# Kernel tuning notes

Hardware: AMD Instinct MI355X
Metric: run time of the kernel (lower is better)

## Reference

```python
import jax, jax.numpy as jnp
import numpy as np

N = 50000
E = 800000
NODE_DIM = 128
EDGE_DIM = 64


def leaky_relu(x, slope=0.2):
    return jnp.where(x >= 0, x, slope * x)


def setup_inputs() -> dict:
    key = jax.random.key(0)
    ks = jax.random.split(key, 12)
    node_feats = jax.random.normal(ks[0], (N, NODE_DIM), dtype=jnp.float32)
    edge_index = jax.random.randint(ks[1], (2, E), 0, N, dtype=jnp.int64)
    edge_feats = jax.random.normal(ks[2], (E, EDGE_DIM), dtype=jnp.float32)
    # msg_mlp: Linear(node+edge -> node), LeakyReLU(0.2), Linear(node -> node)
    s1 = 1.0 / np.sqrt(NODE_DIM + EDGE_DIM)
    s2 = 1.0 / np.sqrt(NODE_DIM)
    s3 = 1.0 / np.sqrt(2 * NODE_DIM)
    msg_w1 = jax.random.uniform(ks[3], (NODE_DIM + EDGE_DIM, NODE_DIM), jnp.float32, -s1, s1)
    msg_b1 = jax.random.uniform(ks[4], (NODE_DIM,), jnp.float32, -s1, s1)
    msg_w2 = jax.random.uniform(ks[5], (NODE_DIM, NODE_DIM), jnp.float32, -s2, s2)
    msg_b2 = jax.random.uniform(ks[6], (NODE_DIM,), jnp.float32, -s2, s2)
    # update_mlp: Linear(2*node -> node), LeakyReLU(0.2), Linear(node -> node)
    upd_w1 = jax.random.uniform(ks[7], (2 * NODE_DIM, NODE_DIM), jnp.float32, -s3, s3)
    upd_b1 = jax.random.uniform(ks[8], (NODE_DIM,), jnp.float32, -s3, s3)
    upd_w2 = jax.random.uniform(ks[9], (NODE_DIM, NODE_DIM), jnp.float32, -s2, s2)
    upd_b2 = jax.random.uniform(ks[10], (NODE_DIM,), jnp.float32, -s2, s2)
    return {
        "node_feats": node_feats,
        "edge_feats": edge_feats,
        "msg_w1": msg_w1, "msg_b1": msg_b1, "msg_w2": msg_w2, "msg_b2": msg_b2,
        "upd_w1": upd_w1, "upd_b1": upd_b1, "upd_w2": upd_w2, "upd_b2": upd_b2,
        "edge_index": edge_index,
    }


def reference(node_feats, edge_feats, msg_w1, msg_b1, msg_w2, msg_b2,
              upd_w1, upd_b1, upd_w2, upd_b2, edge_index):
    src = edge_index[0]
    dst = edge_index[1]
    # gather neighbor features, concat with edge features: (E, node+edge)
    msg_input = jnp.concatenate([node_feats[dst], edge_feats], axis=1)
    h = leaky_relu(msg_input @ msg_w1 + msg_b1)
    messages = h @ msg_w2 + msg_b2                       # (E, node_dim)
    # scatter-add messages to source nodes
    aggregated = jax.ops.segment_sum(messages, src, num_segments=node_feats.shape[0])
    update_input = jnp.concatenate([node_feats, aggregated], axis=1)  # (N, 2*node_dim)
    h2 = leaky_relu(update_input @ upd_w1 + upd_b1)
    return h2 @ upd_w2 + upd_b2                          # (N, node_dim)
```

## Files before the change

### kernel.cpp

```cpp
#include <hip/hip_runtime.h>
#include <hip/hip_bf16.h>

#define NNODES 50000
#define NEDGES 800000
#define NDIM   128
#define EDIM   64
#define K1     192
#define K2     256
#define NB     196

#define KP1 200
#define KPA 136
#define KPU 264
#define MSTR 132

typedef __attribute__((ext_vector_type(8))) short bf16x8;
typedef __attribute__((ext_vector_type(4))) short bf16x4;
typedef __attribute__((ext_vector_type(4))) float f32x4;

__device__ inline short f2bf(float f) {
  union { float f; unsigned u; } v; v.f = f;
  unsigned r = v.u + 0x7FFFu + ((v.u >> 16) & 1u);
  return (short)(r >> 16);
}

__device__ inline bf16x4 pack4(float4 v) {
  bf16x4 p;
  p[0] = f2bf(v.x); p[1] = f2bf(v.y); p[2] = f2bf(v.z); p[3] = f2bf(v.w);
  return p;
}

__global__ __launch_bounds__(256) void cvt_kernel(const float* __restrict__ src,
                                                  short* __restrict__ dst, int n) {
  int i = (blockIdx.x * 256 + threadIdx.x) * 4;
  if (i < n) {
    float4 v = *(const float4*)(src + i);
    *(bf16x4*)(dst + i) = pack4(v);
  }
}

__global__ __launch_bounds__(256) void wt_kernel(const float* __restrict__ w,
                                                 short* __restrict__ wt, int K) {
  int i = blockIdx.x * 256 + threadIdx.x;
  if (i < K * NDIM) {
    int k = i >> 7;
    int n = i & 127;
    wt[n * K + k] = f2bf(w[i]);
  }
}

__global__ __launch_bounds__(256) void hist_kernel(const int* __restrict__ eidx,
                                                   int* __restrict__ cnt) {
  int i = blockIdx.x * 256 + threadIdx.x;
  if (i < NEDGES) atomicAdd(&cnt[eidx[i]], 1);
}

__global__ __launch_bounds__(256) void scan_reduce_kernel(const int* __restrict__ cnt,
                                                          int* __restrict__ bsum) {
  __shared__ int sh[256];
  int tid = threadIdx.x;
  int i = blockIdx.x * 256 + tid;
  sh[tid] = (i < NNODES) ? cnt[i] : 0;
  __syncthreads();
#pragma unroll
  for (int off = 128; off > 0; off >>= 1) {
    if (tid < off) sh[tid] += sh[tid + off];
    __syncthreads();
  }
  if (tid == 0) bsum[blockIdx.x] = sh[0];
}

__global__ __launch_bounds__(256) void scan_top_kernel(const int* __restrict__ bsum,
                                                       int* __restrict__ bscan) {
  __shared__ int sh[256];
  int tid = threadIdx.x;
  int v = (tid < NB) ? bsum[tid] : 0;
  sh[tid] = v;
  __syncthreads();
#pragma unroll
  for (int off = 1; off < 256; off <<= 1) {
    int t = (tid >= off) ? sh[tid - off] : 0;
    __syncthreads();
    sh[tid] += t;
    __syncthreads();
  }
  bscan[tid] = sh[tid] - v;
}

__global__ __launch_bounds__(256) void scan_down_kernel(int* __restrict__ cnt,
                                                        const int* __restrict__ bscan,
                                                        int* __restrict__ row_ptr) {
  __shared__ int sh[256];
  int tid = threadIdx.x;
  int i = blockIdx.x * 256 + tid;
  int v = (i < NNODES) ? cnt[i] : 0;
  sh[tid] = v;
  __syncthreads();
#pragma unroll
  for (int off = 1; off < 256; off <<= 1) {
    int t = (tid >= off) ? sh[tid - off] : 0;
    __syncthreads();
    sh[tid] += t;
    __syncthreads();
  }
  if (i < NNODES) {
    row_ptr[i] = bscan[blockIdx.x] + (sh[tid] - v);
    cnt[i] = 0;
  }
}

__global__ __launch_bounds__(256) void permute_kernel(const int* __restrict__ eidx,
                                                      const int* __restrict__ row_ptr,
                                                      int* __restrict__ cnt,
                                                      int4* __restrict__ s_edges) {
  int e = blockIdx.x * 256 + threadIdx.x;
  if (e < NEDGES) {
    int s = eidx[e];
    int d = eidx[NEDGES + e];
    int pos = row_ptr[s] + atomicAdd(&cnt[s], 1);
    s_edges[pos] = make_int4(s, d, e, 0);
  }
}

__global__ __launch_bounds__(256, 6) void edge_kernel(const short* __restrict__ nf_bf,
                                                      const float* __restrict__ edge_feats,
                                                      const int4* __restrict__ s_edges,
                                                      const short* __restrict__ w1t,
                                                      const float* __restrict__ b1,
                                                      float* __restrict__ hagg) {
  __shared__ __align__(16) char SH[64 * KP1 * 2];
  __shared__ int srcs[64];
  __shared__ int dsts[64];
  __shared__ int eids[64];

  short* X = (short*)SH;
  float* M = (float*)SH;

  const int tid = threadIdx.x;
  const int e0 = blockIdx.x * 64;

  if (tid < 64) {
    int4 v = s_edges[e0 + tid];
    srcs[tid] = v.x;
    dsts[tid] = v.y;
    eids[tid] = v.z;
  }
  __syncthreads();

  {
    int r = tid >> 2, q = tid & 3;
    const bf16x8* np = (const bf16x8*)(nf_bf + (size_t)dsts[r] * NDIM) + q * 4;
    const float4* ep = (const float4*)(edge_feats + (size_t)eids[r] * EDIM) + q * 4;
    short* dpn = X + r * KP1 + q * 32;
    short* dpe = X + r * KP1 + NDIM + q * 16;
#pragma unroll
    for (int j = 0; j < 4; ++j) *(bf16x8*)(dpn + j * 8) = np[j];
#pragma unroll
    for (int j = 0; j < 4; ++j) *(bf16x4*)(dpe + j * 4) = pack4(ep[j]);
  }
  __syncthreads();

  const int lane = tid & 63;
  const int wv = tid >> 6;
  const int m16 = lane & 15;
  const int quad = lane >> 4;

  f32x4 acc[4][2];
#pragma unroll
  for (int mt = 0; mt < 4; ++mt)
#pragma unroll
    for (int nt = 0; nt < 2; ++nt)
      acc[mt][nt] = (f32x4){0.f, 0.f, 0.f, 0.f};

#pragma unroll
  for (int ks = 0; ks < 6; ++ks) {
    const int k0 = ks * 32 + quad * 8;
    bf16x8 b[2];
#pragma unroll
    for (int nt = 0; nt < 2; ++nt) {
      int n = wv * 32 + nt * 16 + m16;
      b[nt] = *(const bf16x8*)(w1t + n * K1 + k0);
    }
#pragma unroll
    for (int mt = 0; mt < 4; ++mt) {
      bf16x8 a = *(const bf16x8*)(X + (mt * 16 + m16) * KP1 + k0);
#pragma unroll
      for (int nt = 0; nt < 2; ++nt)
        acc[mt][nt] = __builtin_amdgcn_mfma_f32_16x16x32_bf16(a, b[nt], acc[mt][nt], 0, 0, 0);
    }
  }
  __syncthreads();

#pragma unroll
  for (int h = 0; h < 2; ++h) {
#pragma unroll
    for (int nt = 0; nt < 2; ++nt) {
      int col = wv * 32 + nt * 16 + m16;
      float bb = b1[col];
#pragma unroll
      for (int mt2 = 0; mt2 < 2; ++mt2) {
        int mt = h * 2 + mt2;
#pragma unroll
        for (int i = 0; i < 4; ++i) {
          float v = acc[mt][nt][i] + bb;
          v = v >= 0.f ? v : 0.2f * v;
          int lr = mt2 * 16 + quad * 4 + i;
          M[lr * MSTR + col] = v;
        }
      }
    }
    __syncthreads();
    {
      const int c = tid & 127;
      const int lr0 = (tid >> 7) * 16;
      const int g0 = h * 32 + lr0;
      float a = M[lr0 * MSTR + c];
      int prev = srcs[g0];
#pragma unroll 4
      for (int r = 1; r < 16; ++r) {
        int s = srcs[g0 + r];
        float v = M[(lr0 + r) * MSTR + c];
        if (s != prev) {
          atomicAdd(&hagg[(size_t)prev * NDIM + c], a);
          a = v;
          prev = s;
        } else {
          a += v;
        }
      }
      atomicAdd(&hagg[(size_t)prev * NDIM + c], a);
    }
    if (h == 0) __syncthreads();
  }
}

__global__ __launch_bounds__(256) void node_kernel(const short* __restrict__ nf_bf,
                                                   const float* __restrict__ hagg,
                                                   const int* __restrict__ degc,
                                                   const short* __restrict__ w2t,
                                                   const float* __restrict__ b2,
                                                   const short* __restrict__ u1t,
                                                   const float* __restrict__ ub1,
                                                   const short* __restrict__ u2t,
                                                   const float* __restrict__ ub2,
                                                   float* __restrict__ out) {
  __shared__ __align__(16) short AGH[64 * KPA];
  __shared__ __align__(16) short XU[64 * KPU];
  __shared__ float degs[64];

  const int tid = threadIdx.x;
  const int n0 = blockIdx.x * 64;

  if (tid < 64) {
    int node = n0 + tid;
    degs[tid] = (node < NNODES) ? (float)degc[node] : 0.f;
  }
  {
    int r = tid >> 2, q = tid & 3;
    int node = n0 + r; if (node >= NNODES) node = NNODES - 1;
    const float4* hp = (const float4*)(hagg + (size_t)node * NDIM) + q * 8;
    const bf16x8* xp = (const bf16x8*)(nf_bf + (size_t)node * NDIM) + q * 4;
    short* ap = AGH + r * KPA + q * 32;
    short* xq = XU + r * KPU + q * 32;
#pragma unroll
    for (int j = 0; j < 8; ++j) *(bf16x4*)(ap + j * 4) = pack4(hp[j]);
#pragma unroll
    for (int j = 0; j < 4; ++j) *(bf16x8*)(xq + j * 8) = xp[j];
  }
  __syncthreads();

  const int lane = tid & 63;
  const int wv = tid >> 6;
  const int m16 = lane & 15;
  const int quad = lane >> 4;

  f32x4 acc[4][2];

#pragma unroll
  for (int mt = 0; mt < 4; ++mt)
#pragma unroll
    for (int nt = 0; nt < 2; ++nt)
      acc[mt][nt] = (f32x4){0.f, 0.f, 0.f, 0.f};
#pragma unroll
  for (int ks = 0; ks < 4; ++ks) {
    const int k0 = ks * 32 + quad * 8;
    bf16x8 b[2];
#pragma unroll
    for (int nt = 0; nt < 2; ++nt) {
      int n = wv * 32 + nt * 16 + m16;
      b[nt] = *(const bf16x8*)(w2t + n * NDIM + k0);
    }
#pragma unroll
    for (int mt = 0; mt < 4; ++mt) {
      bf16x8 a = *(const bf16x8*)(AGH + (mt * 16 + m16) * KPA + k0);
#pragma unroll
      for (int nt = 0; nt < 2; ++nt)
        acc[mt][nt] = __builtin_amdgcn_mfma_f32_16x16x32_bf16(a, b[nt], acc[mt][nt], 0, 0, 0);
    }
  }
#pragma unroll
  for (int nt = 0; nt < 2; ++nt) {
    int col = wv * 32 + nt * 16 + m16;
    float bb = b2[col];
#pragma unroll
    for (int mt = 0; mt < 4; ++mt) {
#pragma unroll
      for (int i = 0; i < 4; ++i) {
        int row = mt * 16 + quad * 4 + i;
        float v = acc[mt][nt][i] + degs[row] * bb;
        XU[row * KPU + NDIM + col] = f2bf(v);
      }
    }
  }
  __syncthreads();

#pragma unroll
  for (int mt = 0; mt < 4; ++mt)
#pragma unroll
    for (int nt = 0; nt < 2; ++nt)
      acc[mt][nt] = (f32x4){0.f, 0.f, 0.f, 0.f};
#pragma unroll
  for (int ks = 0; ks < 8; ++ks) {
    const int k0 = ks * 32 + quad * 8;
    bf16x8 b[2];
#pragma unroll
    for (int nt = 0; nt < 2; ++nt) {
      int n = wv * 32 + nt * 16 + m16;
      b[nt] = *(const bf16x8*)(u1t + n * K2 + k0);
    }
#pragma unroll
    for (int mt = 0; mt < 4; ++mt) {
      bf16x8 a = *(const bf16x8*)(XU + (mt * 16 + m16) * KPU + k0);
#pragma unroll
      for (int nt = 0; nt < 2; ++nt)
        acc[mt][nt] = __builtin_amdgcn_mfma_f32_16x16x32_bf16(a, b[nt], acc[mt][nt], 0, 0, 0);
    }
  }
  __syncthreads();
#pragma unroll
  for (int nt = 0; nt < 2; ++nt) {
    int col = wv * 32 + nt * 16 + m16;
    float bb = ub1[col];
#pragma unroll
    for (int mt = 0; mt < 4; ++mt) {
#pragma unroll
      for (int i = 0; i < 4; ++i) {
        int row = mt * 16 + quad * 4 + i;
        float v = acc[mt][nt][i] + bb;
        v = v >= 0.f ? v : 0.2f * v;
        AGH[row * KPA + col] = f2bf(v);
      }
    }
  }
  __syncthreads();

#pragma unroll
  for (int mt = 0; mt < 4; ++mt)
#pragma unroll
    for (int nt = 0; nt < 2; ++nt)
      acc[mt][nt] = (f32x4){0.f, 0.f, 0.f, 0.f};
#pragma unroll
  for (int ks = 0; ks < 4; ++ks) {
    const int k0 = ks * 32 + quad * 8;
    bf16x8 b[2];
#pragma unroll
    for (int nt = 0; nt < 2; ++nt) {
      int n = wv * 32 + nt * 16 + m16;
      b[nt] = *(const bf16x8*)(u2t + n * NDIM + k0);
    }
#pragma unroll
    for (int mt = 0; mt < 4; ++mt) {
      bf16x8 a = *(const bf16x8*)(AGH + (mt * 16 + m16) * KPA + k0);
#pragma unroll
      for (int nt = 0; nt < 2; ++nt)
        acc[mt][nt] = __builtin_amdgcn_mfma_f32_16x16x32_bf16(a, b[nt], acc[mt][nt], 0, 0, 0);
    }
  }
#pragma unroll
  for (int nt = 0; nt < 2; ++nt) {
    int col = wv * 32 + nt * 16 + m16;
    float bb = ub2[col];
#pragma unroll
    for (int mt = 0; mt < 4; ++mt) {
#pragma unroll
      for (int i = 0; i < 4; ++i) {
        int row = mt * 16 + quad * 4 + i;
        int node = n0 + row;
        if (node < NNODES)
          out[(size_t)node * NDIM + col] = acc[mt][nt][i] + bb;
      }
    }
  }
}

extern "C" void kernel_launch(void* const* d_in, const int* in_sizes, int n_in,
                              void* d_out, int out_size, void* d_ws, size_t ws_size,
                              hipStream_t stream) {
  const float* node_feats = (const float*)d_in[0];
  const float* edge_feats = (const float*)d_in[1];
  const float* msg_w1 = (const float*)d_in[2];
  const float* msg_b1 = (const float*)d_in[3];
  const float* msg_w2 = (const float*)d_in[4];
  const float* msg_b2 = (const float*)d_in[5];
  const float* upd_w1 = (const float*)d_in[6];
  const float* upd_b1 = (const float*)d_in[7];
  const float* upd_w2 = (const float*)d_in[8];
  const float* upd_b2 = (const float*)d_in[9];
  const int* eidx = (const int*)d_in[10];

  float* hagg   = (float*)d_ws;
  int* cnt      = (int*)(hagg + (size_t)NNODES * NDIM);
  int* row_ptr  = cnt + NNODES;
  int* bsum     = row_ptr + NNODES;
  int* bscan    = bsum + 256;
  int4* s_edges = (int4*)(bscan + 256);
  short* w1t    = (short*)(s_edges + NEDGES);
  short* w2t    = w1t + 128 * K1;
  short* u1t    = w2t + 128 * 128;
  short* u2t    = u1t + 128 * K2;
  short* nf_bf  = u2t + 128 * 128;

  hipMemsetAsync(d_ws, 0, (size_t)(NNODES * NDIM + NNODES) * sizeof(float), stream);

  cvt_kernel<<<(NNODES * NDIM / 4 + 255) / 256, 256, 0, stream>>>(node_feats, nf_bf,
                                                                  NNODES * NDIM);
  wt_kernel<<<(K1 * 128) / 256, 256, 0, stream>>>(msg_w1, w1t, K1);
  wt_kernel<<<(128 * 128) / 256, 256, 0, stream>>>(msg_w2, w2t, 128);
  wt_kernel<<<(K2 * 128) / 256, 256, 0, stream>>>(upd_w1, u1t, K2);
  wt_kernel<<<(128 * 128) / 256, 256, 0, stream>>>(upd_w2, u2t, 128);

  hist_kernel<<<NEDGES / 256, 256, 0, stream>>>(eidx, cnt);
  scan_reduce_kernel<<<NB, 256, 0, stream>>>(cnt, bsum);
  scan_top_kernel<<<1, 256, 0, stream>>>(bsum, bscan);
  scan_down_kernel<<<NB, 256, 0, stream>>>(cnt, bscan, row_ptr);
  permute_kernel<<<NEDGES / 256, 256, 0, stream>>>(eidx, row_ptr, cnt, s_edges);

  edge_kernel<<<NEDGES / 64, 256, 0, stream>>>(nf_bf, edge_feats, s_edges,
                                               w1t, msg_b1, hagg);
  node_kernel<<<(NNODES + 63) / 64, 256, 0, stream>>>(nf_bf, hagg, cnt,
                                                      w2t, msg_b2, u1t, upd_b1,
                                                      u2t, upd_b2, (float*)d_out);
}
```

Before: 541.1 us.

## Make edge kernel wave-independent with direct global A-fragment loads

Restructures the edge kernel so each wave owns 32 edges and all 128 output columns. The gathered node and edge features are loaded straight from global memory into MFMA A-fragments, with edge features converted to bf16 in registers, instead of being staged through a shared-memory X tile. Block-wide __syncthreads are replaced with per-wave barriers and an LDS waitcnt. The segmented scatter-add then runs per wave, with each lane handling two columns. This drops the LDS staging and block-level syncs, but doubles the accumulator registers, lowers the occupancy hint from 6 to 3, and makes each wave reload all of W1 from global memory or cache.

```diff
diff --git a/kernel.cpp b/kernel.cpp
--- a/kernel.cpp
+++ b/kernel.cpp
@@ -9,10 +9,11 @@
 #define K2     256
 #define NB     196
 
-#define KP1 200
 #define KPA 136
 #define KPU 264
 #define MSTR 132
+
+#define WAIT_LGKM 0xC07F
 
 typedef __attribute__((ext_vector_type(8))) short bf16x8;
 typedef __attribute__((ext_vector_type(4))) short bf16x4;
@@ -27,6 +28,13 @@
 __device__ inline bf16x4 pack4(float4 v) {
   bf16x4 p;
   p[0] = f2bf(v.x); p[1] = f2bf(v.y); p[2] = f2bf(v.z); p[3] = f2bf(v.w);
+  return p;
+}
+
+__device__ inline bf16x8 pack8(float4 a, float4 b) {
+  bf16x8 p;
+  p[0] = f2bf(a.x); p[1] = f2bf(a.y); p[2] = f2bf(a.z); p[3] = f2bf(a.w);
+  p[4] = f2bf(b.x); p[5] = f2bf(b.y); p[6] = f2bf(b.z); p[7] = f2bf(b.w);
   return p;
 }
 
@@ -122,115 +130,100 @@
   }
 }
 
-__global__ __launch_bounds__(256, 6) void edge_kernel(const short* __restrict__ nf_bf,
+__global__ __launch_bounds__(256, 3) void edge_kernel(const short* __restrict__ nf_bf,
                                                       const float* __restrict__ edge_feats,
                                                       const int4* __restrict__ s_edges,
                                                       const short* __restrict__ w1t,
                                                       const float* __restrict__ b1,
                                                       float* __restrict__ hagg) {
-  __shared__ __align__(16) char SH[64 * KP1 * 2];
-  __shared__ int srcs[64];
-  __shared__ int dsts[64];
-  __shared__ int eids[64];
-
-  short* X = (short*)SH;
-  float* M = (float*)SH;
+  __shared__ __align__(16) float M[4][16 * MSTR];
+  __shared__ int srcs[4][32];
 
   const int tid = threadIdx.x;
-  const int e0 = blockIdx.x * 64;
-
-  if (tid < 64) {
-    int4 v = s_edges[e0 + tid];
-    srcs[tid] = v.x;
-    dsts[tid] = v.y;
-    eids[tid] = v.z;
-  }
-  __syncthreads();
-
-  {
-    int r = tid >> 2, q = tid & 3;
-    const bf16x8* np = (const bf16x8*)(nf_bf + (size_t)dsts[r] * NDIM) + q * 4;
-    const float4* ep = (const float4*)(edge_feats + (size_t)eids[r] * EDIM) + q * 4;
-    short* dpn = X + r * KP1 + q * 32;
-    short* dpe = X + r * KP1 + NDIM + q * 16;
-#pragma unroll
-    for (int j = 0; j < 4; ++j) *(bf16x8*)(dpn + j * 8) = np[j];
-#pragma unroll
-    for (int j = 0; j < 4; ++j) *(bf16x4*)(dpe + j * 4) = pack4(ep[j]);
-  }
-  __syncthreads();
-
+  const int wv = tid >> 6;
   const int lane = tid & 63;
-  const int wv = tid >> 6;
   const int m16 = lane & 15;
   const int quad = lane >> 4;
-
-  f32x4 acc[4][2];
-#pragma unroll
-  for (int mt = 0; mt < 4; ++mt)
-#pragma unroll
-    for (int nt = 0; nt < 2; ++nt)
+  const int g0 = blockIdx.x * 128 + wv * 32;
+
+  int* srcs_w = srcs[wv];
+  float* Mw = M[wv];
+
+  if (lane < 32) srcs_w[lane] = s_edges[g0 + lane].x;
+  const int4 er0 = s_edges[g0 + m16];
+  const int4 er1 = s_edges[g0 + 16 + m16];
+
+  const short* a0n = nf_bf + (size_t)er0.y * NDIM;
+  const short* a1n = nf_bf + (size_t)er1.y * NDIM;
+  const float* a0e = edge_feats + (size_t)er0.z * EDIM;
+  const float* a1e = edge_feats + (size_t)er1.z * EDIM;
+
+  f32x4 acc[2][8];
+#pragma unroll
+  for (int mt = 0; mt < 2; ++mt)
+#pragma unroll
+    for (int nt = 0; nt < 8; ++nt)
       acc[mt][nt] = (f32x4){0.f, 0.f, 0.f, 0.f};
 
 #pragma unroll
   for (int ks = 0; ks < 6; ++ks) {
     const int k0 = ks * 32 + quad * 8;
-    bf16x8 b[2];
-#pragma unroll
-    for (int nt = 0; nt < 2; ++nt) {
-      int n = wv * 32 + nt * 16 + m16;
-      b[nt] = *(const bf16x8*)(w1t + n * K1 + k0);
-    }
-#pragma unroll
-    for (int mt = 0; mt < 4; ++mt) {
-      bf16x8 a = *(const bf16x8*)(X + (mt * 16 + m16) * KP1 + k0);
-#pragma unroll
-      for (int nt = 0; nt < 2; ++nt)
-        acc[mt][nt] = __builtin_amdgcn_mfma_f32_16x16x32_bf16(a, b[nt], acc[mt][nt], 0, 0, 0);
-    }
-  }
-  __syncthreads();
-
-#pragma unroll
-  for (int h = 0; h < 2; ++h) {
-#pragma unroll
-    for (int nt = 0; nt < 2; ++nt) {
-      int col = wv * 32 + nt * 16 + m16;
-      float bb = b1[col];
-#pragma unroll
-      for (int mt2 = 0; mt2 < 2; ++mt2) {
-        int mt = h * 2 + mt2;
-#pragma unroll
-        for (int i = 0; i < 4; ++i) {
-          float v = acc[mt][nt][i] + bb;
-          v = v >= 0.f ? v : 0.2f * v;
-          int lr = mt2 * 16 + quad * 4 + i;
-          M[lr * MSTR + col] = v;
+    bf16x8 a0, a1;
+    if (ks < 4) {
+      a0 = *(const bf16x8*)(a0n + k0);
+      a1 = *(const bf16x8*)(a1n + k0);
+    } else {
+      const int f = k0 - NDIM;
+      a0 = pack8(*(const float4*)(a0e + f), *(const float4*)(a0e + f + 4));
+      a1 = pack8(*(const float4*)(a1e + f), *(const float4*)(a1e + f + 4));
+    }
+#pragma unroll
+    for (int nt = 0; nt < 8; ++nt) {
+      bf16x8 b = *(const bf16x8*)(w1t + (nt * 16 + m16) * K1 + k0);
+      acc[0][nt] = __builtin_amdgcn_mfma_f32_16x16x32_bf16(a0, b, acc[0][nt], 0, 0, 0);
+      acc[1][nt] = __builtin_amdgcn_mfma_f32_16x16x32_bf16(a1, b, acc[1][nt], 0, 0, 0);
+    }
+  }
+
+#pragma unroll
+  for (int mt = 0; mt < 2; ++mt) {
+#pragma unroll
+    for (int nt = 0; nt < 8; ++nt) {
+      const int col = nt * 16 + m16;
+      const float bb = b1[col];
+#pragma unroll
+      for (int i = 0; i < 4; ++i) {
+        float v = acc[mt][nt][i] + bb;
+        v = v >= 0.f ? v : 0.2f * v;
+        Mw[(quad * 4 + i) * MSTR + col] = v;
+      }
+    }
+    __builtin_amdgcn_wave_barrier();
+    __builtin_amdgcn_s_waitcnt(WAIT_LGKM);
+    {
+      const int c0 = lane;
+      const int c1 = lane + 64;
+      int prev = srcs_w[mt * 16];
+      float A0 = Mw[c0];
+      float A1 = Mw[c1];
+#pragma unroll
+      for (int r = 1; r < 16; ++r) {
+        int s = srcs_w[mt * 16 + r];
+        float v0 = Mw[r * MSTR + c0];
+        float v1 = Mw[r * MSTR + c1];
+        if (s != prev) {
+          atomicAdd(&hagg[(size_t)prev * NDIM + c0], A0);
+          atomicAdd(&hagg[(size_t)prev * NDIM + c1], A1);
+          A0 = v0; A1 = v1; prev = s;
+        } else {
+          A0 += v0; A1 += v1;
         }
       }
-    }
-    __syncthreads();
-    {
-      const int c = tid & 127;
-      const int lr0 = (tid >> 7) * 16;
-      const int g0 = h * 32 + lr0;
-      float a = M[lr0 * MSTR + c];
-      int prev = srcs[g0];
-#pragma unroll 4
-      for (int r = 1; r < 16; ++r) {
-        int s = srcs[g0 + r];
-        float v = M[(lr0 + r) * MSTR + c];
-        if (s != prev) {
-          atomicAdd(&hagg[(size_t)prev * NDIM + c], a);
-          a = v;
-          prev = s;
-        } else {
-          a += v;
-        }
-      }
-      atomicAdd(&hagg[(size_t)prev * NDIM + c], a);
-    }
-    if (h == 0) __syncthreads();
+      atomicAdd(&hagg[(size_t)prev * NDIM + c0], A0);
+      atomicAdd(&hagg[(size_t)prev * NDIM + c1], A1);
+    }
+    __builtin_amdgcn_wave_barrier();
+    __builtin_amdgcn_s_waitcnt(WAIT_LGKM);
   }
 }
 
@@ -435,8 +428,8 @@
   scan_down_kernel<<<NB, 256, 0, stream>>>(cnt, bscan, row_ptr);
   permute_kernel<<<NEDGES / 256, 256, 0, stream>>>(eidx, row_ptr, cnt, s_edges);
 
-  edge_kernel<<<NEDGES / 64, 256, 0, stream>>>(nf_bf, edge_feats, s_edges,
-                                               w1t, msg_b1, hagg);
+  edge_kernel<<<NEDGES / 128, 256, 0, stream>>>(nf_bf, edge_feats, s_edges,
+                                                w1t, msg_b1, hagg);
   node_kernel<<<(NNODES + 63) / 64, 256, 0, stream>>>(nf_bf, hagg, cnt,
                                                       w2t, msg_b2, u1t, upd_b1,
                                                       u2t, upd_b2, (float*)d_out);
```

New measurement: 614.1 us. 13.5% more time.
